# Kernel optimization log

Measured on AMD Instinct MI355X. Metric: run time of the kernel, lower is better.

Reference implementation:

```python
import jax, jax.numpy as jnp
import numpy as np

NEG_INF = -1e9  # mask fill; every row has >=1 valid key so softmax is well-defined


def setup_inputs() -> dict:
    B, L, E, A = 4096, 200, 128, 128
    key = jax.random.key(0)
    ks = jax.random.split(key, 8)
    scale = 0.05
    return {
        "query": jax.random.normal(ks[0], (B, E), dtype=jnp.float32),
        "keys": jax.random.normal(ks[1], (B, L, E), dtype=jnp.float32),
        "keys_length": jax.random.randint(ks[2], (B,), 1, L + 1, dtype=jnp.int64),
        "pos_emb": jax.random.normal(ks[3], (L, E), dtype=jnp.float32) * scale,
        "W1": jax.random.normal(ks[4], (4 * E, A), dtype=jnp.float32) * scale,
        "b1": jnp.zeros((A,), dtype=jnp.float32),
        "W2": jax.random.normal(ks[5], (A, A), dtype=jnp.float32) * scale,
        "b2": jnp.zeros((A,), dtype=jnp.float32),
        "W3": jax.random.normal(ks[6], (A, 1), dtype=jnp.float32) * scale,
        "b3": jnp.zeros((1,), dtype=jnp.float32),
    }


def reference(query, keys, keys_length, pos_emb, W1, b1, W2, b2, W3, b3):
    B, L, E = keys.shape
    # add position embedding (positions are simply arange(L) for every batch row)
    keys_p = keys + pos_emb[None, :, :]                      # (B, L, E)
    q = jnp.broadcast_to(query[:, None, :], (B, L, E))       # (B, L, E)
    # DIN attention input: [q, k, q-k, q*k] -> (B, L, 4E)
    att_in = jnp.concatenate([q, keys_p, q - keys_p, q * keys_p], axis=-1)
    h = jax.nn.relu(att_in @ W1 + b1)                        # (B, L, A)
    h = jax.nn.relu(h @ W2 + b2)                             # (B, L, A)
    scores = (h @ W3 + b3)[..., 0]                           # (B, L)
    valid = jnp.arange(L)[None, :] < keys_length[:, None]    # (B, L) bool
    scores = jnp.where(valid, scores, NEG_INF)
    weights = jax.nn.softmax(scores, axis=-1)                # (B, L)
    out = jnp.einsum("bl,ble->be", weights, keys_p)          # (B, E)
    return out
```

## Files before the change

kernel.cpp:

```cpp
#include <hip/hip_runtime.h>
#include <hip/hip_bf16.h>


typedef __attribute__((ext_vector_type(8))) short short8;
typedef __attribute__((ext_vector_type(4))) float f32x4;

__device__ __forceinline__ float bf2f(short s) {
    return __uint_as_float(((unsigned)(unsigned short)s) << 16);
}
__device__ __forceinline__ short f2bf(float f) {
    unsigned u = __float_as_uint(f);
    u = (u + 0x7fff + ((u >> 16) & 1)) >> 16;
    return (short)u;
}

__global__ void prep_frag(const float* __restrict__ W1, const float* __restrict__ W2,
                          short* __restrict__ F1, short* __restrict__ F2) {
    int idx = blockIdx.x * 256 + threadIdx.x;
    if (idx < 4096) {
        int lane = idx & 63, n = (idx >> 6) & 7, kb = idx >> 9;
        int q = lane >> 4, l15 = lane & 15;
        int sp = kb >> 1, half = kb & 1;
        int col = n * 16 + l15;
        short8 v;
        #pragma unroll
        for (int j = 0; j < 8; ++j) {
            int k = 32 * sp + 8 * q + j;
            float x = half ? W1[(384 + k) * 128 + col]
                           : W1[(128 + k) * 128 + col] - W1[(256 + k) * 128 + col];
            v[j] = f2bf(x);
        }
        *(short8*)(F1 + idx * 8) = v;
    } else if (idx < 6144) {
        int i2 = idx - 4096;
        int lane = i2 & 63, n = (i2 >> 6) & 7, s2 = i2 >> 9;
        int q = lane >> 4, l15 = lane & 15;
        int col = n * 16 + l15;
        short8 v;
        #pragma unroll
        for (int j = 0; j < 8; ++j)
            v[j] = f2bf(W2[(32 * s2 + 8 * q + j) * 128 + col]);
        *(short8*)(F2 + i2 * 8) = v;
    }
}

__global__ void prep_qw(const float* __restrict__ query, const float* __restrict__ W1,
                        const float* __restrict__ b1, float* __restrict__ qw) {
    __shared__ float qsh[128];
    const int b = blockIdx.x, t = threadIdx.x;
    qsh[t] = query[b * 128 + t];
    __syncthreads();
    float acc = b1[t];
    #pragma unroll 4
    for (int k = 0; k < 128; ++k)
        acc += qsh[k] * (W1[k * 128 + t] + W1[(256 + k) * 128 + t]);
    qw[b * 128 + t] = acc;
}

#define HSTR 136

__launch_bounds__(256, 2)
__global__ void din_main(const float* __restrict__ query, const float* __restrict__ keys,
                         const int* __restrict__ klen, const float* __restrict__ pos,
                         const float* __restrict__ b2g, const float* __restrict__ w3g,
                         const float* __restrict__ qw, const short* __restrict__ F1,
                         const short* __restrict__ F2, float* __restrict__ out) {
    __shared__ alignas(16) short h1buf[16 * 16 * HSTR];
    __shared__ float qv[128];
    __shared__ float s_lds[208];
    __shared__ float w_lds[208];
    __shared__ float part[512];
    __shared__ float red[8];

    const int t = threadIdx.x;
    const int b = blockIdx.x;
    const int w = t >> 6;
    const int lane = t & 63;
    const int quad = lane >> 4;
    const int l15 = lane & 15;

    const int len = klen[b];
    const int T = (len + 15) >> 4;
    const int cnt = (T > w) ? ((T - w + 3) >> 2) : 0;

    if (t < 128) qv[t] = query[b * 128 + t];
    __syncthreads();

    f32x4 acc[4][8];
    #pragma unroll
    for (int i = 0; i < 4; ++i)
        #pragma unroll
        for (int n = 0; n < 8; ++n) acc[i][n] = (f32x4){0.f, 0.f, 0.f, 0.f};

    if (cnt > 0) {
        for (int sp = 0; sp < 4; ++sp) {
            float4 qa = *(const float4*)(qv + 32 * sp + 8 * quad);
            float4 qb = *(const float4*)(qv + 32 * sp + 8 * quad + 4);
            short8 bf[8];
            #pragma unroll
            for (int n = 0; n < 8; ++n)
                bf[n] = *(const short8*)(F1 + (((2 * sp) * 8 + n) * 64 + lane) * 8);
            short8 af[4];
            #pragma unroll
            for (int i = 0; i < 4; ++i) {
                if (i < cnt) {
                    int row = (w + 4 * i) * 16 + l15;
                    short8 a;
                    if (row < 200) {
                        const float* kr = keys + ((long)b * 200 + row) * 128 + 32 * sp + 8 * quad;
                        const float* pr = pos + (long)row * 128 + 32 * sp + 8 * quad;
                        float4 k0 = *(const float4*)kr, k1 = *(const float4*)(kr + 4);
                        float4 p0 = *(const float4*)pr, p1 = *(const float4*)(pr + 4);
                        a[0] = f2bf(k0.x + p0.x); a[1] = f2bf(k0.y + p0.y);
                        a[2] = f2bf(k0.z + p0.z); a[3] = f2bf(k0.w + p0.w);
                        a[4] = f2bf(k1.x + p1.x); a[5] = f2bf(k1.y + p1.y);
                        a[6] = f2bf(k1.z + p1.z); a[7] = f2bf(k1.w + p1.w);
                    } else {
                        #pragma unroll
                        for (int j = 0; j < 8; ++j) a[j] = 0;
                    }
                    af[i] = a;
                    #pragma unroll
                    for (int n = 0; n < 8; ++n)
                        acc[i][n] = __builtin_amdgcn_mfma_f32_16x16x32_bf16(a, bf[n], acc[i][n], 0, 0, 0);
                }
            }
            #pragma unroll
            for (int n = 0; n < 8; ++n)
                bf[n] = *(const short8*)(F1 + (((2 * sp + 1) * 8 + n) * 64 + lane) * 8);
            #pragma unroll
            for (int i = 0; i < 4; ++i) {
                if (i < cnt) {
                    short8 a;
                    a[0] = f2bf(bf2f(af[i][0]) * qa.x); a[1] = f2bf(bf2f(af[i][1]) * qa.y);
                    a[2] = f2bf(bf2f(af[i][2]) * qa.z); a[3] = f2bf(bf2f(af[i][3]) * qa.w);
                    a[4] = f2bf(bf2f(af[i][4]) * qb.x); a[5] = f2bf(bf2f(af[i][5]) * qb.y);
                    a[6] = f2bf(bf2f(af[i][6]) * qb.z); a[7] = f2bf(bf2f(af[i][7]) * qb.w);
                    #pragma unroll
                    for (int n = 0; n < 8; ++n)
                        acc[i][n] = __builtin_amdgcn_mfma_f32_16x16x32_bf16(a, bf[n], acc[i][n], 0, 0, 0);
                }
            }
        }

        {
            float qwn[8];
            #pragma unroll
            for (int n = 0; n < 8; ++n) qwn[n] = qw[b * 128 + n * 16 + l15];
            #pragma unroll
            for (int i = 0; i < 4; ++i) {
                if (i < cnt) {
                    #pragma unroll
                    for (int n = 0; n < 8; ++n)
                        #pragma unroll
                        for (int r = 0; r < 4; ++r) {
                            float v = acc[i][n][r] + qwn[n];
                            h1buf[((w * 4 + i) * 16 + quad * 4 + r) * HSTR + n * 16 + l15] =
                                f2bf(v > 0.f ? v : 0.f);
                        }
                }
            }
        }

        #pragma unroll
        for (int i = 0; i < 4; ++i)
            #pragma unroll
            for (int n = 0; n < 8; ++n) acc[i][n] = (f32x4){0.f, 0.f, 0.f, 0.f};
        for (int s2 = 0; s2 < 4; ++s2) {
            short8 bf[8];
            #pragma unroll
            for (int n = 0; n < 8; ++n)
                bf[n] = *(const short8*)(F2 + ((s2 * 8 + n) * 64 + lane) * 8);
            #pragma unroll
            for (int i = 0; i < 4; ++i) {
                if (i < cnt) {
                    short8 a = *(const short8*)(h1buf + ((w * 4 + i) * 16 + l15) * HSTR + 32 * s2 + 8 * quad);
                    #pragma unroll
                    for (int n = 0; n < 8; ++n)
                        acc[i][n] = __builtin_amdgcn_mfma_f32_16x16x32_bf16(a, bf[n], acc[i][n], 0, 0, 0);
                }
            }
        }

        {
            float b2n[8], w3n[8];
            #pragma unroll
            for (int n = 0; n < 8; ++n) {
                b2n[n] = b2g[n * 16 + l15];
                w3n[n] = w3g[n * 16 + l15];
            }
            #pragma unroll
            for (int i = 0; i < 4; ++i) {
                if (i < cnt) {
                    float p[4] = {0.f, 0.f, 0.f, 0.f};
                    #pragma unroll
                    for (int n = 0; n < 8; ++n)
                        #pragma unroll
                        for (int r = 0; r < 4; ++r) {
                            float v = acc[i][n][r] + b2n[n];
                            p[r] += (v > 0.f ? v : 0.f) * w3n[n];
                        }
                    #pragma unroll
                    for (int off = 8; off >= 1; off >>= 1)
                        #pragma unroll
                        for (int r = 0; r < 4; ++r) p[r] += __shfl_xor(p[r], off, 64);
                    if (l15 == 0) {
                        #pragma unroll
                        for (int r = 0; r < 4; ++r)
                            s_lds[(w + 4 * i) * 16 + quad * 4 + r] = p[r];
                    }
                }
            }
        }
    }
    __syncthreads();

    float sv = (t < 208 && t < len) ? s_lds[t] : -1e9f;
    float m = sv;
    #pragma unroll
    for (int off = 32; off >= 1; off >>= 1) m = fmaxf(m, __shfl_xor(m, off, 64));
    if (lane == 0) red[w] = m;
    __syncthreads();
    m = fmaxf(fmaxf(red[0], red[1]), fmaxf(red[2], red[3]));
    float e = (t < 208 && t < len) ? expf(sv - m) : 0.f;
    float ssum = e;
    #pragma unroll
    for (int off = 32; off >= 1; off >>= 1) ssum += __shfl_xor(ssum, off, 64);
    if (lane == 0) red[4 + w] = ssum;
    __syncthreads();
    float S = red[4] + red[5] + red[6] + red[7];
    if (t < 208) w_lds[t] = e / S;
    __syncthreads();

    const int qt = t >> 6;
    const int e2h = t & 63;
    float ax = 0.f, ay = 0.f;
    const float2* kr = (const float2*)(keys + (long)b * 200 * 128);
    const float2* pr = (const float2*)pos;
    for (int l = qt; l < len; l += 4) {
        float wgt = w_lds[l];
        float2 kv = kr[l * 64 + e2h];
        float2 pv = pr[l * 64 + e2h];
        ax += wgt * (kv.x + pv.x);
        ay += wgt * (kv.y + pv.y);
    }
    part[qt * 128 + 2 * e2h]     = ax;
    part[qt * 128 + 2 * e2h + 1] = ay;
    __syncthreads();
    if (t < 128) {
        float o = part[t] + part[128 + t] + part[256 + t] + part[384 + t];
        out[b * 128 + t] = o;
    }
}

extern "C" void kernel_launch(void* const* d_in, const int* in_sizes, int n_in,
                              void* d_out, int out_size, void* d_ws, size_t ws_size,
                              hipStream_t stream) {
    const float* query = (const float*)d_in[0];
    const float* keys  = (const float*)d_in[1];
    const int*   klen  = (const int*)  d_in[2];
    const float* pos   = (const float*)d_in[3];
    const float* W1    = (const float*)d_in[4];
    const float* b1    = (const float*)d_in[5];
    const float* W2    = (const float*)d_in[6];
    const float* b2    = (const float*)d_in[7];
    const float* W3    = (const float*)d_in[8];
    float* out = (float*)d_out;

    char* ws = (char*)d_ws;
    float* qw = (float*)ws;
    short* F1 = (short*)(ws + 2097152);
    short* F2 = (short*)(ws + 2097152 + 65536);

    prep_frag<<<24,   256, 0, stream>>>(W1, W2, F1, F2);
    prep_qw  <<<4096, 128, 0, stream>>>(query, W1, b1, qw);
    din_main <<<4096, 256, 0, stream>>>(query, keys, klen, pos, b2, W3, qw,
                                        F1, F2, out);
}
```

Baseline: 715.7 us.

## Split each batch row into 64-key chunks with split-softmax combine kernel

Result: slower. 800.9 us (+11.9%).

```diff
diff --git a/kernel.cpp b/kernel.cpp
--- a/kernel.cpp
+++ b/kernel.cpp
@@ -57,200 +57,187 @@
     qw[b * 128 + t] = acc;
 }
 
-#define HSTR 136
-
-__launch_bounds__(256, 2)
-__global__ void din_main(const float* __restrict__ query, const float* __restrict__ keys,
-                         const int* __restrict__ klen, const float* __restrict__ pos,
-                         const float* __restrict__ b2g, const float* __restrict__ w3g,
-                         const float* __restrict__ qw, const short* __restrict__ F1,
-                         const short* __restrict__ F2, float* __restrict__ out) {
-    __shared__ alignas(16) short h1buf[16 * 16 * HSTR];
-    __shared__ float qv[128];
-    __shared__ float s_lds[208];
-    __shared__ float w_lds[208];
+#define KSTR 136
+
+__launch_bounds__(256, 4)
+__global__ void din_scores(const float* __restrict__ query, const float* __restrict__ keys,
+                           const int* __restrict__ klen, const float* __restrict__ pos,
+                           const float* __restrict__ b2g, const float* __restrict__ w3g,
+                           const float* __restrict__ qw, const short* __restrict__ F1,
+                           const short* __restrict__ F2,
+                           float* __restrict__ Pm, float* __restrict__ Pl,
+                           float* __restrict__ Po) {
+    __shared__ alignas(16) short kpbuf[4 * 16 * KSTR];
+    __shared__ alignas(16) short h1buf[4 * 16 * KSTR];
+    __shared__ float w_e[64];
+    __shared__ float redm[4];
+    __shared__ float redl[4];
     __shared__ float part[512];
-    __shared__ float red[8];
 
     const int t = threadIdx.x;
-    const int b = blockIdx.x;
-    const int w = t >> 6;
-    const int lane = t & 63;
-    const int quad = lane >> 4;
-    const int l15 = lane & 15;
-
+    const int bc = blockIdx.x;
+    const int b = bc >> 2, chunk = bc & 3;
+    const int w = t >> 6, lane = t & 63, quad = lane >> 4, l15 = lane & 15;
     const int len = klen[b];
-    const int T = (len + 15) >> 4;
-    const int cnt = (T > w) ? ((T - w + 3) >> 2) : 0;
-
-    if (t < 128) qv[t] = query[b * 128 + t];
+    const int base = chunk << 6;
+    if (base >= len) {
+        if (t == 0) { Pm[bc] = -1e30f; Pl[bc] = 0.f; }
+        return;
+    }
+    const int rw = base + w * 16;
+    const bool active = (rw < len);
+    short* kpw = kpbuf + w * 16 * KSTR;
+    short* h1w = h1buf + w * 16 * KSTR;
+
+    float sv[4] = {-1e30f, -1e30f, -1e30f, -1e30f};
+
+    if (active) {
+        const int row = rw + l15;
+        float4 K[8];
+        if (row < 200) {
+            const float4* kr = (const float4*)(keys + ((long)b * 200 + row) * 128) + quad * 2;
+            #pragma unroll
+            for (int s = 0; s < 4; ++s) { K[2 * s] = kr[s * 8]; K[2 * s + 1] = kr[s * 8 + 1]; }
+        } else {
+            #pragma unroll
+            for (int j = 0; j < 8; ++j) K[j] = (float4){0.f, 0.f, 0.f, 0.f};
+        }
+
+        f32x4 acc[8];
+        #pragma unroll
+        for (int n = 0; n < 8; ++n) acc[n] = (f32x4){0.f, 0.f, 0.f, 0.f};
+
+        #pragma unroll
+        for (int s = 0; s < 4; ++s) {
+            short8 a;
+            if (row < 200) {
+                const float4* pr = (const float4*)(pos + (long)row * 128) + quad * 2;
+                float4 p0 = pr[s * 8], p1 = pr[s * 8 + 1];
+                float4 k0 = K[2 * s], k1 = K[2 * s + 1];
+                a[0] = f2bf(k0.x + p0.x); a[1] = f2bf(k0.y + p0.y);
+                a[2] = f2bf(k0.z + p0.z); a[3] = f2bf(k0.w + p0.w);
+                a[4] = f2bf(k1.x + p1.x); a[5] = f2bf(k1.y + p1.y);
+                a[6] = f2bf(k1.z + p1.z); a[7] = f2bf(k1.w + p1.w);
+            } else {
+                #pragma unroll
+                for (int j = 0; j < 8; ++j) a[j] = 0;
+            }
+            *(short8*)(kpw + l15 * KSTR + s * 32 + quad * 8) = a;
+            #pragma unroll
+            for (int n = 0; n < 8; ++n) {
+                short8 bf = *(const short8*)(F1 + (((2 * s) * 8 + n) * 64 + lane) * 8);
+                acc[n] = __builtin_amdgcn_mfma_f32_16x16x32_bf16(a, bf, acc[n], 0, 0, 0);
+            }
+            float4 qa = *(const float4*)(query + b * 128 + s * 32 + quad * 8);
+            float4 qb = *(const float4*)(query + b * 128 + s * 32 + quad * 8 + 4);
+            short8 a2;
+            a2[0] = f2bf(bf2f(a[0]) * qa.x); a2[1] = f2bf(bf2f(a[1]) * qa.y);
+            a2[2] = f2bf(bf2f(a[2]) * qa.z); a2[3] = f2bf(bf2f(a[3]) * qa.w);
+            a2[4] = f2bf(bf2f(a[4]) * qb.x); a2[5] = f2bf(bf2f(a[5]) * qb.y);
+            a2[6] = f2bf(bf2f(a[6]) * qb.z); a2[7] = f2bf(bf2f(a[7]) * qb.w);
+            #pragma unroll
+            for (int n = 0; n < 8; ++n) {
+                short8 bf = *(const short8*)(F1 + (((2 * s + 1) * 8 + n) * 64 + lane) * 8);
+                acc[n] = __builtin_amdgcn_mfma_f32_16x16x32_bf16(a2, bf, acc[n], 0, 0, 0);
+            }
+        }
+
+        #pragma unroll
+        for (int n = 0; n < 8; ++n) {
+            float qwn = qw[b * 128 + n * 16 + l15];
+            #pragma unroll
+            for (int r = 0; r < 4; ++r) {
+                float v = acc[n][r] + qwn;
+                h1w[(quad * 4 + r) * KSTR + n * 16 + l15] = f2bf(v > 0.f ? v : 0.f);
+            }
+        }
+
+        #pragma unroll
+        for (int n = 0; n < 8; ++n) acc[n] = (f32x4){0.f, 0.f, 0.f, 0.f};
+        #pragma unroll
+        for (int s2 = 0; s2 < 4; ++s2) {
+            short8 a = *(const short8*)(h1w + l15 * KSTR + s2 * 32 + quad * 8);
+            #pragma unroll
+            for (int n = 0; n < 8; ++n) {
+                short8 bf = *(const short8*)(F2 + ((s2 * 8 + n) * 64 + lane) * 8);
+                acc[n] = __builtin_amdgcn_mfma_f32_16x16x32_bf16(a, bf, acc[n], 0, 0, 0);
+            }
+        }
+
+        float p[4] = {0.f, 0.f, 0.f, 0.f};
+        #pragma unroll
+        for (int n = 0; n < 8; ++n) {
+            float b2n = b2g[n * 16 + l15];
+            float w3n = w3g[n * 16 + l15];
+            #pragma unroll
+            for (int r = 0; r < 4; ++r) {
+                float v = acc[n][r] + b2n;
+                p[r] += (v > 0.f ? v : 0.f) * w3n;
+            }
+        }
+        #pragma unroll
+        for (int off = 8; off >= 1; off >>= 1) {
+            #pragma unroll
+            for (int r = 0; r < 4; ++r) p[r] += __shfl_xor(p[r], off, 64);
+        }
+        #pragma unroll
+        for (int r = 0; r < 4; ++r)
+            sv[r] = (rw + quad * 4 + r < len) ? p[r] : -1e30f;
+    }
+
+    float m = fmaxf(fmaxf(sv[0], sv[1]), fmaxf(sv[2], sv[3]));
+    m = fmaxf(m, __shfl_xor(m, 16, 64));
+    m = fmaxf(m, __shfl_xor(m, 32, 64));
+    if (lane == 0) redm[w] = m;
     __syncthreads();
-
-    f32x4 acc[4][8];
+    const float M = fmaxf(fmaxf(redm[0], redm[1]), fmaxf(redm[2], redm[3]));
+    float e[4], esum = 0.f;
     #pragma unroll
-    for (int i = 0; i < 4; ++i)
-        #pragma unroll
-        for (int n = 0; n < 8; ++n) acc[i][n] = (f32x4){0.f, 0.f, 0.f, 0.f};
-
-    if (cnt > 0) {
-        for (int sp = 0; sp < 4; ++sp) {
-            float4 qa = *(const float4*)(qv + 32 * sp + 8 * quad);
-            float4 qb = *(const float4*)(qv + 32 * sp + 8 * quad + 4);
-            short8 bf[8];
-            #pragma unroll
-            for (int n = 0; n < 8; ++n)
-                bf[n] = *(const short8*)(F1 + (((2 * sp) * 8 + n) * 64 + lane) * 8);
-            short8 af[4];
-            #pragma unroll
-            for (int i = 0; i < 4; ++i) {
-                if (i < cnt) {
-                    int row = (w + 4 * i) * 16 + l15;
-                    short8 a;
-                    if (row < 200) {
-                        const float* kr = keys + ((long)b * 200 + row) * 128 + 32 * sp + 8 * quad;
-                        const float* pr = pos + (long)row * 128 + 32 * sp + 8 * quad;
-                        float4 k0 = *(const float4*)kr, k1 = *(const float4*)(kr + 4);
-                        float4 p0 = *(const float4*)pr, p1 = *(const float4*)(pr + 4);
-                        a[0] = f2bf(k0.x + p0.x); a[1] = f2bf(k0.y + p0.y);
-                        a[2] = f2bf(k0.z + p0.z); a[3] = f2bf(k0.w + p0.w);
-                        a[4] = f2bf(k1.x + p1.x); a[5] = f2bf(k1.y + p1.y);
-                        a[6] = f2bf(k1.z + p1.z); a[7] = f2bf(k1.w + p1.w);
-                    } else {
-                        #pragma unroll
-                        for (int j = 0; j < 8; ++j) a[j] = 0;
-                    }
-                    af[i] = a;
-                    #pragma unroll
-                    for (int n = 0; n < 8; ++n)
-                        acc[i][n] = __builtin_amdgcn_mfma_f32_16x16x32_bf16(a, bf[n], acc[i][n], 0, 0, 0);
-                }
-            }
-            #pragma unroll
-            for (int n = 0; n < 8; ++n)
-                bf[n] = *(const short8*)(F1 + (((2 * sp + 1) * 8 + n) * 64 + lane) * 8);
-            #pragma unroll
-            for (int i = 0; i < 4; ++i) {
-                if (i < cnt) {
-                    short8 a;
-                    a[0] = f2bf(bf2f(af[i][0]) * qa.x); a[1] = f2bf(bf2f(af[i][1]) * qa.y);
-                    a[2] = f2bf(bf2f(af[i][2]) * qa.z); a[3] = f2bf(bf2f(af[i][3]) * qa.w);
-                    a[4] = f2bf(bf2f(af[i][4]) * qb.x); a[5] = f2bf(bf2f(af[i][5]) * qb.y);
-                    a[6] = f2bf(bf2f(af[i][6]) * qb.z); a[7] = f2bf(bf2f(af[i][7]) * qb.w);
-                    #pragma unroll
-                    for (int n = 0; n < 8; ++n)
-                        acc[i][n] = __builtin_amdgcn_mfma_f32_16x16x32_bf16(a, bf[n], acc[i][n], 0, 0, 0);
-                }
-            }
-        }
-
-        {
-            float qwn[8];
-            #pragma unroll
-            for (int n = 0; n < 8; ++n) qwn[n] = qw[b * 128 + n * 16 + l15];
-            #pragma unroll
-            for (int i = 0; i < 4; ++i) {
-                if (i < cnt) {
-                    #pragma unroll
-                    for (int n = 0; n < 8; ++n)
-                        #pragma unroll
-                        for (int r = 0; r < 4; ++r) {
-                            float v = acc[i][n][r] + qwn[n];
-                            h1buf[((w * 4 + i) * 16 + quad * 4 + r) * HSTR + n * 16 + l15] =
-                                f2bf(v > 0.f ? v : 0.f);
-                        }
-                }
-            }
-        }
-
-        #pragma unroll
-        for (int i = 0; i < 4; ++i)
-            #pragma unroll
-            for (int n = 0; n < 8; ++n) acc[i][n] = (f32x4){0.f, 0.f, 0.f, 0.f};
-        for (int s2 = 0; s2 < 4; ++s2) {
-            short8 bf[8];
-            #pragma unroll
-            for (int n = 0; n < 8; ++n)
-                bf[n] = *(const short8*)(F2 + ((s2 * 8 + n) * 64 + lane) * 8);
-            #pragma unroll
-            for (int i = 0; i < 4; ++i) {
-                if (i < cnt) {
-                    short8 a = *(const short8*)(h1buf + ((w * 4 + i) * 16 + l15) * HSTR + 32 * s2 + 8 * quad);
-                    #pragma unroll
-                    for (int n = 0; n < 8; ++n)
-                        acc[i][n] = __builtin_amdgcn_mfma_f32_16x16x32_bf16(a, bf[n], acc[i][n], 0, 0, 0);
-                }
-            }
-        }
-
-        {
-            float b2n[8], w3n[8];
-            #pragma unroll
-            for (int n = 0; n < 8; ++n) {
-                b2n[n] = b2g[n * 16 + l15];
-                w3n[n] = w3g[n * 16 + l15];
-            }
-            #pragma unroll
-            for (int i = 0; i < 4; ++i) {
-                if (i < cnt) {
-                    float p[4] = {0.f, 0.f, 0.f, 0.f};
-                    #pragma unroll
-                    for (int n = 0; n < 8; ++n)
-                        #pragma unroll
-                        for (int r = 0; r < 4; ++r) {
-                            float v = acc[i][n][r] + b2n[n];
-                            p[r] += (v > 0.f ? v : 0.f) * w3n[n];
-                        }
-                    #pragma unroll
-                    for (int off = 8; off >= 1; off >>= 1)
-                        #pragma unroll
-                        for (int r = 0; r < 4; ++r) p[r] += __shfl_xor(p[r], off, 64);
-                    if (l15 == 0) {
-                        #pragma unroll
-                        for (int r = 0; r < 4; ++r)
-                            s_lds[(w + 4 * i) * 16 + quad * 4 + r] = p[r];
-                    }
-                }
-            }
-        }
-    }
+    for (int r = 0; r < 4; ++r) {
+        e[r] = (sv[r] > -1e29f) ? __expf(sv[r] - M) : 0.f;
+        esum += e[r];
+    }
+    esum += __shfl_xor(esum, 16, 64);
+    esum += __shfl_xor(esum, 32, 64);
+    if (lane == 0) redl[w] = esum;
+    if (active && l15 == 0) {
+        #pragma unroll
+        for (int r = 0; r < 4; ++r) w_e[w * 16 + quad * 4 + r] = e[r];
+    }
+    float ax = 0.f, ay = 0.f;
+    if (active) {
+        #pragma unroll
+        for (int j = 0; j < 16; ++j) {
+            float wj = w_e[w * 16 + j];
+            unsigned pr = *(const unsigned*)(kpw + j * KSTR + lane * 2);
+            ax += wj * __uint_as_float(pr << 16);
+            ay += wj * __uint_as_float(pr & 0xffff0000u);
+        }
+    }
+    part[w * 128 + lane * 2]     = ax;
+    part[w * 128 + lane * 2 + 1] = ay;
     __syncthreads();
-
-    float sv = (t < 208 && t < len) ? s_lds[t] : -1e9f;
-    float m = sv;
-    #pragma unroll
-    for (int off = 32; off >= 1; off >>= 1) m = fmaxf(m, __shfl_xor(m, off, 64));
-    if (lane == 0) red[w] = m;
-    __syncthreads();
-    m = fmaxf(fmaxf(red[0], red[1]), fmaxf(red[2], red[3]));
-    float e = (t < 208 && t < len) ? expf(sv - m) : 0.f;
-    float ssum = e;
-    #pragma unroll
-    for (int off = 32; off >= 1; off >>= 1) ssum += __shfl_xor(ssum, off, 64);
-    if (lane == 0) red[4 + w] = ssum;
-    __syncthreads();
-    float S = red[4] + red[5] + red[6] + red[7];
-    if (t < 208) w_lds[t] = e / S;
-    __syncthreads();
-
-    const int qt = t >> 6;
-    const int e2h = t & 63;
-    float ax = 0.f, ay = 0.f;
-    const float2* kr = (const float2*)(keys + (long)b * 200 * 128);
-    const float2* pr = (const float2*)pos;
-    for (int l = qt; l < len; l += 4) {
-        float wgt = w_lds[l];
-        float2 kv = kr[l * 64 + e2h];
-        float2 pv = pr[l * 64 + e2h];
-        ax += wgt * (kv.x + pv.x);
-        ay += wgt * (kv.y + pv.y);
-    }
-    part[qt * 128 + 2 * e2h]     = ax;
-    part[qt * 128 + 2 * e2h + 1] = ay;
-    __syncthreads();
-    if (t < 128) {
-        float o = part[t] + part[128 + t] + part[256 + t] + part[384 + t];
-        out[b * 128 + t] = o;
-    }
+    if (t < 128)
+        Po[bc * 128 + t] = part[t] + part[128 + t] + part[256 + t] + part[384 + t];
+    if (t == 0) {
+        Pm[bc] = M;
+        Pl[bc] = redl[0] + redl[1] + redl[2] + redl[3];
+    }
+}
+
+__global__ void din_combine(const float* __restrict__ Pm, const float* __restrict__ Pl,
+                            const float* __restrict__ Po, float* __restrict__ out) {
+    const int b = blockIdx.x, t = threadIdx.x;
+    const float m0 = Pm[b * 4], m1 = Pm[b * 4 + 1], m2 = Pm[b * 4 + 2], m3 = Pm[b * 4 + 3];
+    const float M = fmaxf(fmaxf(m0, m1), fmaxf(m2, m3));
+    const float w0 = (m0 > -1e29f) ? __expf(m0 - M) : 0.f;
+    const float w1 = (m1 > -1e29f) ? __expf(m1 - M) : 0.f;
+    const float w2 = (m2 > -1e29f) ? __expf(m2 - M) : 0.f;
+    const float w3 = (m3 > -1e29f) ? __expf(m3 - M) : 0.f;
+    const float S = w0 * Pl[b * 4] + w1 * Pl[b * 4 + 1] + w2 * Pl[b * 4 + 2] + w3 * Pl[b * 4 + 3];
+    float o = w0 * Po[(b * 4) * 128 + t] + w1 * Po[(b * 4 + 1) * 128 + t]
+            + w2 * Po[(b * 4 + 2) * 128 + t] + w3 * Po[(b * 4 + 3) * 128 + t];
+    out[b * 128 + t] = o / S;
 }
 
 extern "C" void kernel_launch(void* const* d_in, const int* in_sizes, int n_in,
@@ -271,9 +258,13 @@
     float* qw = (float*)ws;
     short* F1 = (short*)(ws + 2097152);
     short* F2 = (short*)(ws + 2097152 + 65536);
-
-    prep_frag<<<24,   256, 0, stream>>>(W1, W2, F1, F2);
-    prep_qw  <<<4096, 128, 0, stream>>>(query, W1, b1, qw);
-    din_main <<<4096, 256, 0, stream>>>(query, keys, klen, pos, b2, W3, qw,
-                                        F1, F2, out);
-}
+    float* Pm = (float*)(ws + 2097152 + 98304);
+    float* Pl = (float*)(ws + 2097152 + 163840);
+    float* Po = (float*)(ws + 2097152 + 229376);
+
+    prep_frag  <<<24,    256, 0, stream>>>(W1, W2, F1, F2);
+    prep_qw    <<<4096,  128, 0, stream>>>(query, W1, b1, qw);
+    din_scores <<<16384, 256, 0, stream>>>(query, keys, klen, pos, b2, W3, qw,
+                                           F1, F2, Pm, Pl, Po);
+    din_combine<<<4096,  128, 0, stream>>>(Pm, Pl, Po, out);
+}
```
